# Kernel tuning notes

Measured on AMD Instinct MI355X. Metric: run time of the kernel, lower is better.

Reference implementation:

```python
import jax, jax.numpy as jnp
import numpy as np
from jax import lax

UNITS = [100, 80, 50, 30]
IN_FEAT = 64

def setup_inputs() -> dict:
    key = jax.random.key(0)
    ks = jax.random.split(key, 16)
    B, T, F = 512, 512, IN_FEAT
    ins = [F] + UNITS[:-1]
    d = {"x": jax.random.normal(ks[0], (B, T, F), jnp.float32)}
    for li, (u, fi) in enumerate(zip(UNITS, ins)):
        din = u + fi  # concat([h, x]) per the cell
        scale = 1.0 / np.sqrt(din)
        d[f"W{li}"] = jax.random.normal(ks[1 + li], (din, 4 * u), jnp.float32) * scale
        d[f"b{li}"] = jnp.zeros((4 * u,), jnp.float32)
    d["Wout"] = jax.random.normal(ks[10], (UNITS[-1], 1), jnp.float32) * (1.0 / np.sqrt(UNITS[-1]))
    d["bout"] = jnp.zeros((1,), jnp.float32)
    return d

def _lstm_layer(x, W, b, units, return_sequences):
    # x: [B, T, F] -> hidden sequence [B, T, units] or last hidden [B, units]
    B = x.shape[0]
    h0 = jnp.zeros((B, units), x.dtype)
    c0 = jnp.zeros((B, units), x.dtype)

    def step(carry, xt):
        h, c = carry
        z = jnp.concatenate([h, xt], axis=-1) @ W + b  # [B, 4u]
        f, i, g, o = jnp.split(z, 4, axis=-1)  # gate order: forget, input, candidate, output
        f = jax.nn.sigmoid(f)
        i = jax.nn.sigmoid(i)
        g = jnp.tanh(g)
        c_new = f * c + i * g
        h_new = jax.nn.sigmoid(o) * jnp.tanh(c_new)
        return (h_new, c_new), (h_new if return_sequences else None)

    xs = jnp.swapaxes(x, 0, 1)  # [T, B, F]
    (h_last, _), hs = lax.scan(step, (h0, c0), xs)
    if return_sequences:
        return jnp.swapaxes(hs, 0, 1)  # [B, T, units]
    return h_last

def reference(x, W0, b0, W1, b1, W2, b2, W3, b3, Wout, bout):
    # Dropout layers are identity at inference (training=False).
    h = _lstm_layer(x, W0, b0, UNITS[0], True)
    h = _lstm_layer(h, W1, b1, UNITS[1], True)
    h = _lstm_layer(h, W2, b2, UNITS[2], True)
    h = _lstm_layer(h, W3, b3, UNITS[3], False)  # last-layer RNN returns final hidden only
    return h @ Wout + bout  # [B, 1]
```

## Files before the change

### kernel.cpp

```cpp
#include <hip/hip_runtime.h>


#define T_SEQ 512
#define B_TOT 512

__device__ __forceinline__ float sigmoidf_(float x) {
    return 1.0f / (1.0f + __expf(-x));
}
__device__ __forceinline__ float tanh_fast(float x) {
    float e = __expf(2.0f * x);
    return 1.0f - 2.0f / (1.0f + e);
}

template<int U, int FI, int S, int JT, int BLOCK, bool SEQ, bool FINAL>
__global__ __launch_bounds__(BLOCK)
void lstm_layer(const float* __restrict__ X,
                const float* __restrict__ W,
                const float* __restrict__ Bv,
                float* __restrict__ Hout,
                const float* __restrict__ Wd,
                const float* __restrict__ bd,
                float* __restrict__ OUT)
{
    constexpr int DIN  = U + FI;
    constexpr int DIN4 = ((DIN + 4*S - 1) / (4*S)) * (4*S);
    constexpr int KH   = DIN4 / S;
    constexpr int G    = 4 * U;
    constexpr int NP   = G / JT;
    constexpr int NT   = NP * S;

    __shared__ __align__(16) float in0[DIN4];
    __shared__ __align__(16) float in1[DIN4];
    __shared__ __align__(16) float zp[S * 2 * G];

    const int tid = threadIdx.x;
    const int bb  = blockIdx.x * 2;

    const int p = tid % NP;
    const int s = tid / NP;
    float w[JT][KH];
    if (tid < NT) {
        #pragma unroll
        for (int c = 0; c < JT; ++c) {
            #pragma unroll
            for (int kk = 0; kk < KH; ++kk) {
                const int k = s * KH + kk;
                w[c][kk] = (k < DIN) ? W[(size_t)k * G + (JT * p + c)] : 0.0f;
            }
        }
    }

    const int cb = (tid < 2*U) ? (tid / U) : 0;
    const int cu = (tid < 2*U) ? (tid - cb*U) : 0;
    float gbf = 0, gbi = 0, gbg = 0, gbo = 0, creg = 0.0f;
    if (tid < 2*U) {
        gbf = Bv[cu]; gbi = Bv[cu + U]; gbg = Bv[cu + 2*U]; gbo = Bv[cu + 3*U];
    }
    float* myin = cb ? in1 : in0;

    const int xb = (tid < 2*FI) ? (tid / FI) : 0;
    const int xk = (tid < 2*FI) ? (tid - xb*FI) : 0;
    const float* Xrow = X + (size_t)(bb + xb) * T_SEQ * FI + xk;
    float* xin = xb ? in1 : in0;

    for (int k = tid; k < DIN4; k += BLOCK) {
        if (k < U || k >= U + FI) { in0[k] = 0.0f; in1[k] = 0.0f; }
    }
    if (tid < 2*FI) xin[U + xk] = Xrow[0];
    __syncthreads();

    const float4* f40 = (const float4*)in0;
    const float4* f41 = (const float4*)in1;
    const int qbase = s * (KH / 4);

    for (int t = 0; t < T_SEQ; ++t) {
        float xpre = 0.0f;
        const bool do_x = (tid < 2*FI) && (t + 1 < T_SEQ);
        if (do_x) xpre = Xrow[(size_t)(t + 1) * FI];

        if (tid < NT) {
            float acc[JT][2];
            #pragma unroll
            for (int c = 0; c < JT; ++c) { acc[c][0] = 0.0f; acc[c][1] = 0.0f; }
            #pragma unroll
            for (int q = 0; q < KH/4; ++q) {
                const float4 av = f40[qbase + q];
                const float4 bv = f41[qbase + q];
                #pragma unroll
                for (int c = 0; c < JT; ++c) {
                    acc[c][0] += w[c][4*q+0] * av.x; acc[c][1] += w[c][4*q+0] * bv.x;
                    acc[c][0] += w[c][4*q+1] * av.y; acc[c][1] += w[c][4*q+1] * bv.y;
                    acc[c][0] += w[c][4*q+2] * av.z; acc[c][1] += w[c][4*q+2] * bv.z;
                    acc[c][0] += w[c][4*q+3] * av.w; acc[c][1] += w[c][4*q+3] * bv.w;
                }
            }
            float* z0 = &zp[(s*2 + 0) * G + JT * p];
            float* z1 = &zp[(s*2 + 1) * G + JT * p];
            #pragma unroll
            for (int c = 0; c < JT; ++c) { z0[c] = acc[c][0]; z1[c] = acc[c][1]; }
        }
        __syncthreads();

        if (tid < 2*U) {
            float zf = gbf, zi = gbi, zg = gbg, zo = gbo;
            #pragma unroll
            for (int s2 = 0; s2 < S; ++s2) {
                const float* zr = &zp[(s2*2 + cb) * G];
                zf += zr[cu]; zi += zr[cu + U]; zg += zr[cu + 2*U]; zo += zr[cu + 3*U];
            }
            const float fg = sigmoidf_(zf);
            const float ig = sigmoidf_(zi);
            const float gg = tanh_fast(zg);
            const float og = sigmoidf_(zo);
            creg = fg * creg + ig * gg;
            const float hn = og * tanh_fast(creg);
            myin[cu] = hn;
            if constexpr (SEQ) {
                Hout[((size_t)(bb + cb) * T_SEQ + t) * U + cu] = hn;
            }
        }
        if (do_x) xin[U + xk] = xpre;
        __syncthreads();
    }

    if constexpr (FINAL) {
        if (tid < 2) {
            const float* hh = tid ? in1 : in0;
            float acc = bd[0];
            #pragma unroll
            for (int u2 = 0; u2 < U; ++u2) acc += hh[u2] * Wd[u2];
            OUT[bb + tid] = acc;
        }
    }
}

extern "C" void kernel_launch(void* const* d_in, const int* in_sizes, int n_in,
                              void* d_out, int out_size, void* d_ws, size_t ws_size,
                              hipStream_t stream)
{
    const float* x    = (const float*)d_in[0];
    const float* W0   = (const float*)d_in[1];
    const float* b0   = (const float*)d_in[2];
    const float* W1   = (const float*)d_in[3];
    const float* b1   = (const float*)d_in[4];
    const float* W2   = (const float*)d_in[5];
    const float* b2   = (const float*)d_in[6];
    const float* W3   = (const float*)d_in[7];
    const float* b3   = (const float*)d_in[8];
    const float* Wout = (const float*)d_in[9];
    const float* bout = (const float*)d_in[10];
    float* out = (float*)d_out;

    float* H0 = (float*)d_ws;
    float* H1 = H0 + (size_t)B_TOT * T_SEQ * 100;
    float* H2 = (float*)d_ws;

    const dim3 grid(B_TOT / 2);

    hipLaunchKernelGGL((lstm_layer<100,  64, 4, 4, 448, true,  false>),
                       grid, dim3(448), 0, stream, x,  W0, b0, H0, nullptr, nullptr, nullptr);
    hipLaunchKernelGGL((lstm_layer< 80, 100, 4, 2, 640, true,  false>),
                       grid, dim3(640), 0, stream, H0, W1, b1, H1, nullptr, nullptr, nullptr);
    hipLaunchKernelGGL((lstm_layer< 50,  80, 4, 2, 448, true,  false>),
                       grid, dim3(448), 0, stream, H1, W2, b2, H2, nullptr, nullptr, nullptr);
    hipLaunchKernelGGL((lstm_layer< 30,  50, 4, 2, 256, false, true >),
                       grid, dim3(256), 0, stream, H2, W3, b3, nullptr, Wout, bout, out);
}
```

Before: 2.261 ms.

## Reduce LSTM gate partials with warp shuffles and double-buffer inputs to drop a barrier

Each thread now owns all four gates of one hidden unit across an 8-way K split. Partial sums are reduced with xor-shuffles inside the wavefront instead of through shared memory plus a second barrier, so every thread holds the full gate values and applies the cell update redundantly. Inputs are laid out interleaved for both batch rows in a double-buffered, padded shared array. Dedicated loader threads prefetch the next timestep's x, leaving one __syncthreads per step. The cost is larger blocks, more weight registers per thread (4×KH), and duplicated activation math.

```diff
diff --git a/kernel.cpp b/kernel.cpp
--- a/kernel.cpp
+++ b/kernel.cpp
@@ -12,7 +12,7 @@
     return 1.0f - 2.0f / (1.0f + e);
 }
 
-template<int U, int FI, int S, int JT, int BLOCK, bool SEQ, bool FINAL>
+template<int U, int FI, int KH, int BLOCK, bool SEQ, bool FINAL>
 __global__ __launch_bounds__(BLOCK)
 void lstm_layer(const float* __restrict__ X,
                 const float* __restrict__ W,
@@ -22,113 +22,133 @@
                 const float* __restrict__ bd,
                 float* __restrict__ OUT)
 {
+    constexpr int S    = 8;
     constexpr int DIN  = U + FI;
-    constexpr int DIN4 = ((DIN + 4*S - 1) / (4*S)) * (4*S);
-    constexpr int KH   = DIN4 / S;
-    constexpr int G    = 4 * U;
-    constexpr int NP   = G / JT;
-    constexpr int NT   = NP * S;
+    constexpr int DIN4 = KH * S;
+    static_assert(DIN4 >= DIN, "k-padding must cover DIN");
+    static_assert((KH & 1) == 0, "KH even: each float4 = 2 interleaved k");
+    constexpr int G  = 4 * U;
+    constexpr int NT = U * S;
+    static_assert(NT <= BLOCK, "GEMV threads must fit");
+    constexpr int ST0    = (2 * KH + 3) / 4 * 4;
+    constexpr int STRIDE = (ST0 % 8 == 4) ? ST0 : ST0 + 4;
+    constexpr int TOT    = STRIDE * S;
 
-    __shared__ __align__(16) float in0[DIN4];
-    __shared__ __align__(16) float in1[DIN4];
-    __shared__ __align__(16) float zp[S * 2 * G];
+    __shared__ __align__(16) float buf[2][TOT];
 
     const int tid = threadIdx.x;
     const int bb  = blockIdx.x * 2;
 
-    const int p = tid % NP;
-    const int s = tid / NP;
-    float w[JT][KH];
+    const int p = tid >> 3;
+    const int s = tid & 7;
+
+    float w[4][KH];
+    float bia[4] = {0.f, 0.f, 0.f, 0.f};
     if (tid < NT) {
         #pragma unroll
-        for (int c = 0; c < JT; ++c) {
+        for (int g = 0; g < 4; ++g) {
             #pragma unroll
             for (int kk = 0; kk < KH; ++kk) {
                 const int k = s * KH + kk;
-                w[c][kk] = (k < DIN) ? W[(size_t)k * G + (JT * p + c)] : 0.0f;
+                w[g][kk] = (k < DIN) ? W[(size_t)k * G + g * U + p] : 0.0f;
+            }
+            if (s == 0) bia[g] = Bv[g * U + p];
+        }
+    }
+
+    const int roff4 = (s * STRIDE) >> 2;
+    const int hidx = (p / KH) * STRIDE + 2 * (p % KH);
+
+    const int nload = BLOCK - NT;
+    const int lidx  = tid - NT;
+
+    for (int i = tid; i < 2 * TOT; i += BLOCK) ((float*)buf)[i] = 0.0f;
+    __syncthreads();
+    if (tid >= NT) {
+        #pragma unroll
+        for (int rep = 0; rep < 2; ++rep) {
+            const int j = lidx + rep * nload;
+            if (j < 2 * FI) {
+                const int r  = (j < FI) ? 0 : 1;
+                const int jj = j - r * FI;
+                const int k  = U + jj;
+                const int wi = (k / KH) * STRIDE + 2 * (k % KH) + r;
+                buf[0][wi] = X[(size_t)(bb + r) * T_SEQ * FI + jj];
             }
         }
     }
-
-    const int cb = (tid < 2*U) ? (tid / U) : 0;
-    const int cu = (tid < 2*U) ? (tid - cb*U) : 0;
-    float gbf = 0, gbi = 0, gbg = 0, gbo = 0, creg = 0.0f;
-    if (tid < 2*U) {
-        gbf = Bv[cu]; gbi = Bv[cu + U]; gbg = Bv[cu + 2*U]; gbo = Bv[cu + 3*U];
-    }
-    float* myin = cb ? in1 : in0;
-
-    const int xb = (tid < 2*FI) ? (tid / FI) : 0;
-    const int xk = (tid < 2*FI) ? (tid - xb*FI) : 0;
-    const float* Xrow = X + (size_t)(bb + xb) * T_SEQ * FI + xk;
-    float* xin = xb ? in1 : in0;
-
-    for (int k = tid; k < DIN4; k += BLOCK) {
-        if (k < U || k >= U + FI) { in0[k] = 0.0f; in1[k] = 0.0f; }
-    }
-    if (tid < 2*FI) xin[U + xk] = Xrow[0];
     __syncthreads();
 
-    const float4* f40 = (const float4*)in0;
-    const float4* f41 = (const float4*)in1;
-    const int qbase = s * (KH / 4);
+    float h[2] = {0.f, 0.f}, c[2] = {0.f, 0.f};
 
     for (int t = 0; t < T_SEQ; ++t) {
-        float xpre = 0.0f;
-        const bool do_x = (tid < 2*FI) && (t + 1 < T_SEQ);
-        if (do_x) xpre = Xrow[(size_t)(t + 1) * FI];
+        const int cur = t & 1, nxt = cur ^ 1;
 
         if (tid < NT) {
-            float acc[JT][2];
+            float acc[4][2];
             #pragma unroll
-            for (int c = 0; c < JT; ++c) { acc[c][0] = 0.0f; acc[c][1] = 0.0f; }
+            for (int g = 0; g < 4; ++g) { acc[g][0] = bia[g]; acc[g][1] = bia[g]; }
+            const float4* rb = (const float4*)&buf[cur][0];
             #pragma unroll
-            for (int q = 0; q < KH/4; ++q) {
-                const float4 av = f40[qbase + q];
-                const float4 bv = f41[qbase + q];
+            for (int q = 0; q < KH / 2; ++q) {
+                const float4 v = rb[roff4 + q];
                 #pragma unroll
-                for (int c = 0; c < JT; ++c) {
-                    acc[c][0] += w[c][4*q+0] * av.x; acc[c][1] += w[c][4*q+0] * bv.x;
-                    acc[c][0] += w[c][4*q+1] * av.y; acc[c][1] += w[c][4*q+1] * bv.y;
-                    acc[c][0] += w[c][4*q+2] * av.z; acc[c][1] += w[c][4*q+2] * bv.z;
-                    acc[c][0] += w[c][4*q+3] * av.w; acc[c][1] += w[c][4*q+3] * bv.w;
+                for (int g = 0; g < 4; ++g) {
+                    acc[g][0] += w[g][2*q]   * v.x;
+                    acc[g][1] += w[g][2*q]   * v.y;
+                    acc[g][0] += w[g][2*q+1] * v.z;
+                    acc[g][1] += w[g][2*q+1] * v.w;
                 }
             }
-            float* z0 = &zp[(s*2 + 0) * G + JT * p];
-            float* z1 = &zp[(s*2 + 1) * G + JT * p];
             #pragma unroll
-            for (int c = 0; c < JT; ++c) { z0[c] = acc[c][0]; z1[c] = acc[c][1]; }
-        }
-        __syncthreads();
-
-        if (tid < 2*U) {
-            float zf = gbf, zi = gbi, zg = gbg, zo = gbo;
+            for (int m = 1; m < 8; m <<= 1) {
+                #pragma unroll
+                for (int g = 0; g < 4; ++g) {
+                    acc[g][0] += __shfl_xor(acc[g][0], m, 64);
+                    acc[g][1] += __shfl_xor(acc[g][1], m, 64);
+                }
+            }
             #pragma unroll
-            for (int s2 = 0; s2 < S; ++s2) {
-                const float* zr = &zp[(s2*2 + cb) * G];
-                zf += zr[cu]; zi += zr[cu + U]; zg += zr[cu + 2*U]; zo += zr[cu + 3*U];
+            for (int r = 0; r < 2; ++r) {
+                const float F  = sigmoidf_(acc[0][r]);
+                const float I  = sigmoidf_(acc[1][r]);
+                const float Gv = tanh_fast(acc[2][r]);
+                const float O  = sigmoidf_(acc[3][r]);
+                c[r] = F * c[r] + I * Gv;
+                h[r] = O * tanh_fast(c[r]);
             }
-            const float fg = sigmoidf_(zf);
-            const float ig = sigmoidf_(zi);
-            const float gg = tanh_fast(zg);
-            const float og = sigmoidf_(zo);
-            creg = fg * creg + ig * gg;
-            const float hn = og * tanh_fast(creg);
-            myin[cu] = hn;
+            if (s == 0) {
+                *(float2*)&buf[nxt][hidx] = make_float2(h[0], h[1]);
+            }
             if constexpr (SEQ) {
-                Hout[((size_t)(bb + cb) * T_SEQ + t) * U + cu] = hn;
+                if (s == 2) Hout[((size_t)bb       * T_SEQ + t) * U + p] = h[0];
+                if (s == 3) Hout[((size_t)(bb + 1) * T_SEQ + t) * U + p] = h[1];
+            }
+        } else if (t + 1 < T_SEQ) {
+            #pragma unroll
+            for (int rep = 0; rep < 2; ++rep) {
+                const int j = lidx + rep * nload;
+                if (j < 2 * FI) {
+                    const int r  = (j < FI) ? 0 : 1;
+                    const int jj = j - r * FI;
+                    const int k  = U + jj;
+                    const int wi = (k / KH) * STRIDE + 2 * (k % KH) + r;
+                    buf[nxt][wi] = X[(size_t)(bb + r) * T_SEQ * FI + (size_t)(t + 1) * FI + jj];
+                }
             }
         }
-        if (do_x) xin[U + xk] = xpre;
         __syncthreads();
     }
 
     if constexpr (FINAL) {
+        if (tid < NT && s == 0) {
+            buf[0][2 * p]     = h[0] * Wd[p];
+            buf[0][2 * p + 1] = h[1] * Wd[p];
+        }
+        __syncthreads();
         if (tid < 2) {
-            const float* hh = tid ? in1 : in0;
             float acc = bd[0];
-            #pragma unroll
-            for (int u2 = 0; u2 < U; ++u2) acc += hh[u2] * Wd[u2];
+            for (int u = 0; u < U; ++u) acc += buf[0][2 * u + tid];
             OUT[bb + tid] = acc;
         }
     }
@@ -157,12 +177,12 @@
 
     const dim3 grid(B_TOT / 2);
 
-    hipLaunchKernelGGL((lstm_layer<100,  64, 4, 4, 448, true,  false>),
-                       grid, dim3(448), 0, stream, x,  W0, b0, H0, nullptr, nullptr, nullptr);
-    hipLaunchKernelGGL((lstm_layer< 80, 100, 4, 2, 640, true,  false>),
-                       grid, dim3(640), 0, stream, H0, W1, b1, H1, nullptr, nullptr, nullptr);
-    hipLaunchKernelGGL((lstm_layer< 50,  80, 4, 2, 448, true,  false>),
-                       grid, dim3(448), 0, stream, H1, W2, b2, H2, nullptr, nullptr, nullptr);
-    hipLaunchKernelGGL((lstm_layer< 30,  50, 4, 2, 256, false, true >),
-                       grid, dim3(256), 0, stream, H2, W3, b3, nullptr, Wout, bout, out);
+    hipLaunchKernelGGL((lstm_layer<100,  64, 22, 960, true,  false>),
+                       grid, dim3(960), 0, stream, x,  W0, b0, H0, nullptr, nullptr, nullptr);
+    hipLaunchKernelGGL((lstm_layer< 80, 100, 24, 768, true,  false>),
+                       grid, dim3(768), 0, stream, H0, W1, b1, H1, nullptr, nullptr, nullptr);
+    hipLaunchKernelGGL((lstm_layer< 50,  80, 18, 512, true,  false>),
+                       grid, dim3(512), 0, stream, H1, W2, b2, H2, nullptr, nullptr, nullptr);
+    hipLaunchKernelGGL((lstm_layer< 30,  50, 10, 384, false, true >),
+                       grid, dim3(384), 0, stream, H2, W3, b3, nullptr, Wout, bout, out);
 }
```

Result: slower. 3.982 ms (+76.1%).
